# Kernel tuning notes

Hardware: AMD Instinct MI355X
Metric: run time of the kernel (lower is better)

The kernel has to match this reference:

```python
import jax, jax.numpy as jnp
import numpy as np

N, Lq, Lk = 4, 4096, 4096
H, P = 16, 128
D = H * P  # 2048


def setup_inputs() -> dict:
    key = jax.random.key(0)
    ks = jax.random.split(key, 7)
    s = 1.0 / np.sqrt(D).astype(np.float32)
    query = jax.random.normal(ks[0], (N, Lq, D), jnp.float32)
    key_t = jax.random.normal(ks[1], (N, Lk, D), jnp.float32)
    Wq = jax.random.normal(ks[2], (D, D), jnp.float32) * s
    Wk = jax.random.normal(ks[3], (D, D), jnp.float32) * s
    Wv = jax.random.normal(ks[4], (D, D), jnp.float32) * s
    query_padding_mask = jax.random.uniform(ks[5], (N, Lq)) < 0.1
    key_padding_mask = jax.random.uniform(ks[6], (N, Lk)) < 0.1
    return {"query": query, "key": key_t, "Wq": Wq, "Wk": Wk, "Wv": Wv,
            "query_padding_mask": query_padding_mask,
            "key_padding_mask": key_padding_mask}


def reference(query, key, Wq, Wk, Wv, query_padding_mask, key_padding_mask):
    n, lq, _ = query.shape
    lk = key.shape[1]
    # torch.nn.Linear(bias=False): y = x @ W^T; split into heads -> (N,H,L,P)
    q = (query @ Wq.T).reshape(n, lq, H, P).transpose(0, 2, 1, 3)
    k = (key @ Wk.T).reshape(n, lk, H, P).transpose(0, 2, 1, 3)
    v = (key @ Wv.T).reshape(n, lk, H, P).transpose(0, 2, 1, 3)
    # _log_exp_kernel(x) = log(1 + exp(x)) = softplus
    pq = jax.nn.softplus(q)
    pk = jax.nn.softplus(k)
    # zero out padded keys so they contribute nothing to numerator/denominator
    pk = jnp.where(key_padding_mask[:, None, :, None], 0.0, pk)
    # linear attention: O(L*d^2) instead of O(L^2*d)
    kv = jnp.einsum("nhkd,nhke->nhde", pk, v)          # (N,H,P,P)
    num = jnp.einsum("nhqd,nhde->nhqe", pq, kv)        # (N,H,Lq,P)
    den = jnp.einsum("nhqd,nhd->nhq", pq, pk.sum(axis=2))[..., None]
    att = num / den
    out = att.transpose(0, 2, 1, 3).reshape(n, lq, H * P)
    # zero out padded query positions
    out = jnp.where(query_padding_mask[..., None], 0.0, out)
    return out
```

## Files before the change

kernel.cpp:

```cpp
#include <hip/hip_runtime.h>
#include <stdint.h>

typedef __attribute__((ext_vector_type(8))) short    bh8;
typedef __attribute__((ext_vector_type(4))) float    fx4;
typedef __attribute__((ext_vector_type(4))) float    f4v;
typedef unsigned short u16;
typedef __attribute__((ext_vector_type(4))) unsigned short u16x4;

#define DEV static __device__ __forceinline__

DEV u16 f2bf(float f) {
  unsigned u = __float_as_uint(f);
  u += 0x7FFFu + ((u >> 16) & 1u);
  return (u16)(u >> 16);
}
DEV float bf2f(u16 s) { return __uint_as_float(((unsigned)s) << 16); }
DEV float softplus_f(float x) { return fmaxf(x, 0.f) + log1pf(expf(-fabsf(x))); }

DEV void gload_lds16(const u16* g, u16* l) {
  __builtin_amdgcn_global_load_lds(
      (const __attribute__((address_space(1))) unsigned int*)g,
      (__attribute__((address_space(3))) unsigned int*)l, 16, 0, 0);
}
DEV void stage2(const u16* s, u16* d) {
  gload_lds16(s, d);
  gload_lds16(s + 131072, d + 4096);
}

__global__ __launch_bounds__(256) void k_cvt(const float* __restrict__ in,
                                             u16* __restrict__ out, int n4) {
  int i = blockIdx.x * 256 + threadIdx.x;
  int stride = gridDim.x * 256;
  for (; i < n4; i += stride) {
    f4v v = ((const f4v*)in)[i];
    u16x4 o;
    o.x = f2bf(v.x); o.y = f2bf(v.y); o.z = f2bf(v.z); o.w = f2bf(v.w);
    ((u16x4*)out)[i] = o;
  }
}


#define MM(a, b, c) __builtin_amdgcn_mfma_f32_16x16x32_bf16(a, b, c, 0, 0, 0)
#define LD(BASE, RR, KS) \
  (*(const bh8*)&lsg[(BASE) + (RR) * 64 + ((((KS) * 32) + ko8) ^ swz)])

#define DECLQ(Q)                                                          \
  fx4 acc##Q##00 = {}, acc##Q##01 = {}, acc##Q##10 = {}, acc##Q##11 = {}, \
      acc##Q##20 = {}, acc##Q##21 = {}, acc##Q##30 = {}, acc##Q##31 = {}

#define WL asm volatile("s_waitcnt lgkmcnt(0)")
#define WV asm volatile("s_waitcnt vmcnt(4)"); asm volatile("s_waitcnt lgkmcnt(0)")

#define LDA4(AB, KS)                                                     \
  a_0##KS = LD(AB, arow0,      KS); a_1##KS = LD(AB, arow0 + 16, KS);    \
  a_2##KS = LD(AB, arow0 + 32, KS); a_3##KS = LD(AB, arow0 + 48, KS);

#define LDB2(BN, BB, KS)                                                 \
  b##BN##_0##KS = LD(BB, brow0,      KS);                                \
  b##BN##_1##KS = LD(BB, brow0 + 16, KS);

#define MFMA8(Q, BN, KS)                                                 \
  acc##Q##00 = MM(a_0##KS, b##BN##_0##KS, acc##Q##00);                   \
  acc##Q##01 = MM(a_0##KS, b##BN##_1##KS, acc##Q##01);                   \
  acc##Q##10 = MM(a_1##KS, b##BN##_0##KS, acc##Q##10);                   \
  acc##Q##11 = MM(a_1##KS, b##BN##_1##KS, acc##Q##11);                   \
  acc##Q##20 = MM(a_2##KS, b##BN##_0##KS, acc##Q##20);                   \
  acc##Q##21 = MM(a_2##KS, b##BN##_1##KS, acc##Q##21);                   \
  acc##Q##30 = MM(a_3##KS, b##BN##_0##KS, acc##Q##30);                   \
  acc##Q##31 = MM(a_3##KS, b##BN##_1##KS, acc##Q##31);

#define PHASE(MFMAS, WAITS, SSRC, SDST, ...) {  \
  __VA_ARGS__                                   \
  stage2(SSRC, SDST);                           \
  __builtin_amdgcn_s_barrier();                 \
  __builtin_amdgcn_s_setprio(1);                \
  MFMAS                                         \
  __builtin_amdgcn_s_setprio(0);                \
  WAITS;                                        \
  __builtin_amdgcn_s_barrier();                 \
}

#define STE(AC, EL, JOFF) {                                                   \
  float v = AC.EL;                                                            \
  if (EPI >= 1) v = softplus_f(v);                                            \
  if (EPI == 2) { if (mask[gi0 + JOFF]) v = 0.f; }                            \
  C[(size_t)(gi0 + JOFF) * 2048 + gj] = f2bf(v);                              \
}
#define ST1(AC, QR, QC, MI, NI) {                                             \
  int gi0 = bm0 + (QR) * 128 + wr * 64 + (MI) * 16 + (lane >> 4) * 4;         \
  int gj  = bn0 + (QC) * 128 + wc * 32 + (NI) * 16 + l15;                     \
  STE(AC, x, 0) STE(AC, y, 1) STE(AC, z, 2) STE(AC, w, 3)                     \
}
#define EPIQ(Q, QR, QC)                                                       \
  ST1(acc##Q##00, QR, QC, 0, 0) ST1(acc##Q##01, QR, QC, 0, 1)                 \
  ST1(acc##Q##10, QR, QC, 1, 0) ST1(acc##Q##11, QR, QC, 1, 1)                 \
  ST1(acc##Q##20, QR, QC, 2, 0) ST1(acc##Q##21, QR, QC, 2, 1)                 \
  ST1(acc##Q##30, QR, QC, 3, 0) ST1(acc##Q##31, QR, QC, 3, 1)

template <int EPI>
__global__ __launch_bounds__(512, 2) void k_gemm256(
    const u16* __restrict__ A, const u16* __restrict__ B, u16* __restrict__ C,
    const int* __restrict__ mask) {
  extern __shared__ u16 lsg[];
  int tid = threadIdx.x, lane = tid & 63, wid = tid >> 6;
  int xcd = blockIdx.x & 7, i = blockIdx.x >> 3;
  int bm0 = (xcd * 8 + (i & 7)) << 8;
  int bn0 = (i >> 3) << 8;
  int wr = wid >> 2, wc = wid & 3;
  int l15 = lane & 15, ko8 = (lane >> 4) * 8;
  int swz = (l15 & 7) << 3;
  int arow0 = wr * 64 + l15, brow0 = wc * 32 + l15;
  int lr = lane >> 3, cg = (lane & 7) ^ lr;
  const u16* srcA = A + (size_t)(bm0 + wid * 8 + lr) * 2048 + cg * 8;
  const u16* srcB = B + (size_t)(bn0 + wid * 8 + lr) * 2048 + cg * 8;
  u16* lsu = lsg + wid * 512;

  DECLQ(0); DECLQ(1); DECLQ(2); DECLQ(3);
  bh8 a_00 = {}, a_01 = {}, a_10 = {}, a_11 = {},
      a_20 = {}, a_21 = {}, a_30 = {}, a_31 = {};
  bh8 b0_00 = {}, b0_01 = {}, b0_10 = {}, b0_11 = {};
  bh8 b1_00 = {}, b1_01 = {}, b1_10 = {}, b1_11 = {};

  stage2(srcA, lsu + 0);
  stage2(srcB, lsu + 16384);
  stage2(srcA + 262144, lsu + 8192);
  stage2(srcB + 262144, lsu + 24576);
  stage2(srcA + 64, lsu + 32768);
  stage2(srcB + 64, lsu + 49152);
  asm volatile("s_waitcnt vmcnt(4)");
  __builtin_amdgcn_s_barrier();

  for (int it = 0; it < 16; it++) {
    int t1 = 2 * it + 1;
    int t2 = (2 * it + 2) & 31;
    int t3 = (2 * it + 3) & 31;
    PHASE(MFMA8(0, 0, 0) MFMA8(1, 1, 0), WL,
          srcA + 262144 + t1 * 64, lsu + 40960,
          LDA4(0, 0) LDB2(0, 16384, 0) LDB2(1, 24576, 0))
    PHASE(MFMA8(0, 0, 1) MFMA8(1, 1, 1), WL,
          srcB + 262144 + t1 * 64, lsu + 57344,
          LDA4(0, 1) LDB2(0, 16384, 1) LDB2(1, 24576, 1))
    PHASE(MFMA8(2, 0, 0) MFMA8(3, 1, 0), WL,
          srcA + t2 * 64, lsu + 0,
          LDA4(8192, 0))
    PHASE(MFMA8(2, 0, 1) MFMA8(3, 1, 1), WV,
          srcB + t2 * 64, lsu + 16384,
          LDA4(8192, 1))
    PHASE(MFMA8(0, 0, 0) MFMA8(1, 1, 0), WL,
          srcA + 262144 + t2 * 64, lsu + 8192,
          LDA4(32768, 0) LDB2(0, 49152, 0) LDB2(1, 57344, 0))
    PHASE(MFMA8(0, 0, 1) MFMA8(1, 1, 1), WL,
          srcB + 262144 + t2 * 64, lsu + 24576,
          LDA4(32768, 1) LDB2(0, 49152, 1) LDB2(1, 57344, 1))
    PHASE(MFMA8(2, 0, 0) MFMA8(3, 1, 0), WL,
          srcA + t3 * 64, lsu + 32768,
          LDA4(40960, 0))
    PHASE(MFMA8(2, 0, 1) MFMA8(3, 1, 1), WV,
          srcB + t3 * 64, lsu + 49152,
          LDA4(40960, 1))
  }

  EPIQ(0, 0, 0)
  EPIQ(1, 0, 1)
  EPIQ(2, 1, 0)
  EPIQ(3, 1, 1)
}

__global__ __launch_bounds__(256, 2) void k_kv2(const u16* __restrict__ pk,
                                                const u16* __restrict__ v,
                                                float* __restrict__ part,
                                                float* __restrict__ spart) {
  int nh = blockIdx.x >> 3, slab = blockIdx.x & 7;
  int n = nh >> 4, h = nh & 15;
  __shared__ u16 lsA[128 * 32];
  __shared__ u16 lsB[128 * 32];
  __shared__ float redS[32][128];
  int tid = threadIdx.x, lane = tid & 63, wid = tid >> 6;
  int wr = wid >> 1, wc = wid & 1;
  int kk = tid >> 3;
  int dg = (tid & 7) * 16;
  size_t rowbase = ((size_t)(n * 4096 + slab * 512) + kk) * 2048 + h * 128 + dg;
  int r = lane & 15, ko = (lane >> 4) * 8;
  fx4 acc[4][4] = {};
  float sA[16];
#pragma unroll
  for (int i = 0; i < 16; i++) sA[i] = 0.f;
  for (int k0 = 0; k0 < 512; k0 += 32) {
    __syncthreads();
    bh8 a0 = *(const bh8*)(pk + rowbase + (size_t)k0 * 2048);
    bh8 a1 = *(const bh8*)(pk + rowbase + (size_t)k0 * 2048 + 8);
    bh8 b0 = *(const bh8*)(v + rowbase + (size_t)k0 * 2048);
    bh8 b1 = *(const bh8*)(v + rowbase + (size_t)k0 * 2048 + 8);
#pragma unroll
    for (int i = 0; i < 8; i++) {
      sA[i] += bf2f((u16)a0[i]);
      sA[8 + i] += bf2f((u16)a1[i]);
    }
#pragma unroll
    for (int i = 0; i < 8; i++) {
      lsA[(dg + i) * 32 + kk] = (u16)a0[i];
      lsA[(dg + 8 + i) * 32 + kk] = (u16)a1[i];
      lsB[(dg + i) * 32 + kk] = (u16)b0[i];
      lsB[(dg + 8 + i) * 32 + kk] = (u16)b1[i];
    }
    __syncthreads();
    bh8 af[4], bfr[4];
#pragma unroll
    for (int mi = 0; mi < 4; mi++)
      af[mi] = *(const bh8*)&lsA[(wr * 64 + mi * 16 + r) * 32 + ko];
#pragma unroll
    for (int ni = 0; ni < 4; ni++)
      bfr[ni] = *(const bh8*)&lsB[(wc * 64 + ni * 16 + r) * 32 + ko];
#pragma unroll
    for (int mi = 0; mi < 4; mi++)
#pragma unroll
      for (int ni = 0; ni < 4; ni++)
        acc[mi][ni] = __builtin_amdgcn_mfma_f32_16x16x32_bf16(af[mi], bfr[ni],
                                                              acc[mi][ni], 0, 0, 0);
  }
#pragma unroll
  for (int mi = 0; mi < 4; mi++)
#pragma unroll
    for (int ni = 0; ni < 4; ni++)
#pragma unroll
      for (int j = 0; j < 4; j++) {
        int d = wr * 64 + mi * 16 + (lane >> 4) * 4 + j;
        int e = wc * 64 + ni * 16 + (lane & 15);
        part[(size_t)blockIdx.x * 16384 + e * 128 + d] = acc[mi][ni][j];
      }
#pragma unroll
  for (int i = 0; i < 16; i++) redS[kk][dg + i] = sA[i];
  __syncthreads();
  if (tid < 128) {
    float s = 0.f;
#pragma unroll
    for (int p = 0; p < 32; p++) s += redS[p][tid];
    spart[blockIdx.x * 128 + tid] = s;
  }
}

__global__ __launch_bounds__(256) void k_red(const float* __restrict__ part,
                                             const float* __restrict__ spart,
                                             u16* __restrict__ kvT,
                                             float* __restrict__ sb) {
  int nh = blockIdx.x, tid = threadIdx.x;
  for (int i = tid; i < 16384; i += 256) {
    float s = 0.f;
#pragma unroll
    for (int sl = 0; sl < 8; sl++) s += part[(size_t)(nh * 8 + sl) * 16384 + i];
    kvT[(size_t)nh * 16384 + i] = f2bf(s);
  }
  if (tid < 128) {
    float s = 0.f;
#pragma unroll
    for (int sl = 0; sl < 8; sl++) s += spart[(nh * 8 + sl) * 128 + tid];
    sb[nh * 128 + tid] = s;
  }
}

__global__ __launch_bounds__(256, 2) void k_att(
    const u16* __restrict__ pq, const u16* __restrict__ kvT,
    const float* __restrict__ s, const int* __restrict__ qmask,
    float* __restrict__ out) {
  int b = blockIdx.x;
  int lt = b & 31, h = (b >> 5) & 15, nb = b >> 9;
  int l0 = lt * 128;
  __shared__ u16 lsQ[128 * 128];
  __shared__ u16 lsKV[128 * 128];
  __shared__ float lsS[128];
  __shared__ float lsDen[128];
  int tid = threadIdx.x, lane = tid & 63, wid = tid >> 6;

  int row = tid >> 1, part = tid & 1;
  const u16* gq = pq + ((size_t)(nb * 4096 + l0 + row)) * 2048 + h * 128 + part * 64;
  const u16* gk = kvT + ((size_t)(nb * 16 + h) * 128 + row) * 128 + part * 64;
  int sw = (row & 7) << 3;
#pragma unroll
  for (int j = 0; j < 8; j++) {
    bh8 vq = *(const bh8*)(gq + j * 8);
    bh8 vk = *(const bh8*)(gk + j * 8);
    int ci = (part * 64 + j * 8) ^ sw;
    *(bh8*)&lsQ[row * 128 + ci] = vq;
    *(bh8*)&lsKV[row * 128 + ci] = vk;
  }
  if (tid < 128) lsS[tid] = s[(nb * 16 + h) * 128 + tid];
  __syncthreads();

  if (tid < 128) {
    int rr = tid, swr = (rr & 7) << 3;
    float dsum = 0.f;
    for (int dd = 0; dd < 128; dd++) {
      int d = (dd + rr) & 127;
      dsum += bf2f(lsQ[rr * 128 + (d ^ swr)]) * lsS[d];
    }
    lsDen[rr] = dsum;
  }
  __syncthreads();

  int wr = wid >> 1, wc = wid & 1;
  int r = lane & 15, ko = (lane >> 4) * 8;
  fx4 acc[4][4] = {};
#pragma unroll
  for (int ks = 0; ks < 4; ks++) {
    bh8 af[4], bfr[4];
#pragma unroll
    for (int mi = 0; mi < 4; mi++) {
      int rw = wr * 64 + mi * 16 + r;
      af[mi] = *(const bh8*)&lsQ[rw * 128 + ((ks * 32 + ko) ^ ((rw & 7) << 3))];
    }
#pragma unroll
    for (int ni = 0; ni < 4; ni++) {
      int rw = wc * 64 + ni * 16 + r;
      bfr[ni] = *(const bh8*)&lsKV[rw * 128 + ((ks * 32 + ko) ^ ((rw & 7) << 3))];
    }
#pragma unroll
    for (int mi = 0; mi < 4; mi++)
#pragma unroll
      for (int ni = 0; ni < 4; ni++)
        acc[mi][ni] = __builtin_amdgcn_mfma_f32_16x16x32_bf16(af[mi], bfr[ni],
                                                              acc[mi][ni], 0, 0, 0);
  }
#pragma unroll
  for (int mi = 0; mi < 4; mi++)
#pragma unroll
    for (int ni = 0; ni < 4; ni++)
#pragma unroll
      for (int j = 0; j < 4; j++) {
        int li = wr * 64 + mi * 16 + (lane >> 4) * 4 + j;
        int e = wc * 64 + ni * 16 + (lane & 15);
        int l = l0 + li;
        float v = qmask[nb * 4096 + l] ? 0.f : acc[mi][ni][j] / lsDen[li];
        out[((size_t)(nb * 4096 + l)) * 2048 + h * 128 + e] = v;
      }
}

extern "C" void kernel_launch(void* const* d_in, const int* in_sizes, int n_in,
                              void* d_out, int out_size, void* d_ws, size_t ws_size,
                              hipStream_t stream) {
  const float* query = (const float*)d_in[0];
  const float* key   = (const float*)d_in[1];
  const float* Wq    = (const float*)d_in[2];
  const float* Wk    = (const float*)d_in[3];
  const float* Wv    = (const float*)d_in[4];
  const int* qmask   = (const int*)d_in[5];
  const int* kmask   = (const int*)d_in[6];
  float* out = (float*)d_out;
  char* ws = (char*)d_ws;

  u16* qb   = (u16*)(ws + 0);
  u16* kb   = (u16*)(ws + 67108864ull);
  u16* Wqb  = (u16*)(ws + 134217728ull);
  u16* Wkb  = (u16*)(ws + 142606336ull);
  u16* Wvb  = (u16*)(ws + 150994944ull);
  u16* pq   = (u16*)(ws + 159383552ull);
  u16* kvT  = (u16*)(ws + 226492416ull);
  float* sb = (float*)(ws + 228589568ull);
  float* kvpart = (float*)(ws + 0);
  float* spart  = (float*)(ws + 33554432ull);
  u16* pk = (u16*)d_out;
  u16* vb = (u16*)d_out + 33554432ull;

  k_cvt<<<2048, 256, 0, stream>>>(query, qb, 33554432 / 4);
  k_cvt<<<2048, 256, 0, stream>>>(key, kb, 33554432 / 4);
  k_cvt<<<512, 256, 0, stream>>>(Wq, Wqb, 4194304 / 4);
  k_cvt<<<512, 256, 0, stream>>>(Wk, Wkb, 4194304 / 4);
  k_cvt<<<512, 256, 0, stream>>>(Wv, Wvb, 4194304 / 4);

  k_gemm256<1><<<512, 512, 131072, stream>>>(qb, Wqb, pq, nullptr);
  k_gemm256<2><<<512, 512, 131072, stream>>>(kb, Wkb, pk, kmask);
  k_gemm256<0><<<512, 512, 131072, stream>>>(kb, Wvb, vb, nullptr);

  k_kv2<<<512, 256, 0, stream>>>(pk, vb, kvpart, spart);
  k_red<<<64, 256, 0, stream>>>(kvpart, spart, kvT, sb);
  k_att<<<2048, 256, 0, stream>>>(pq, kvT, sb, qmask, out);
}
```

Measured before the change: 739.1 us.

## Software-pipeline LDS fragment loads one phase ahead of MFMAs in GEMM

Restructures the 8-phase GEMM main loop so each phase issues the LDS fragment reads for the next phase's MFMAs, and moves the global-to-LDS staging into reordered slots. The per-phase lgkmcnt(0) waits are dropped and replaced by vmcnt(6)/vmcnt(4) waits on global loads. The prologue now stages an extra tile and preloads the first fragments. The aim is to hide LDS read latency behind MFMA execution. The cost is more live fragment registers and a tighter buffer-reuse schedule that is hard to verify for races.

Result: no change. 741.5 us (+0.3%).

```diff
diff --git a/kernel.cpp b/kernel.cpp
--- a/kernel.cpp
+++ b/kernel.cpp
@@ -48,8 +48,9 @@
   fx4 acc##Q##00 = {}, acc##Q##01 = {}, acc##Q##10 = {}, acc##Q##11 = {}, \
       acc##Q##20 = {}, acc##Q##21 = {}, acc##Q##30 = {}, acc##Q##31 = {}
 
-#define WL asm volatile("s_waitcnt lgkmcnt(0)")
-#define WV asm volatile("s_waitcnt vmcnt(4)"); asm volatile("s_waitcnt lgkmcnt(0)")
+#define WN
+#define WV6 asm volatile("s_waitcnt vmcnt(6)");
+#define WV4 asm volatile("s_waitcnt vmcnt(4)");
 
 #define LDA4(AB, KS)                                                     \
   a_0##KS = LD(AB, arow0,      KS); a_1##KS = LD(AB, arow0 + 16, KS);    \
@@ -69,14 +70,13 @@
   acc##Q##30 = MM(a_3##KS, b##BN##_0##KS, acc##Q##30);                   \
   acc##Q##31 = MM(a_3##KS, b##BN##_1##KS, acc##Q##31);
 
-#define PHASE(MFMAS, WAITS, SSRC, SDST, ...) {  \
+#define PH(MFMAS, WAITS, ...) {                 \
   __VA_ARGS__                                   \
-  stage2(SSRC, SDST);                           \
   __builtin_amdgcn_s_barrier();                 \
   __builtin_amdgcn_s_setprio(1);                \
   MFMAS                                         \
   __builtin_amdgcn_s_setprio(0);                \
-  WAITS;                                        \
+  WAITS                                         \
   __builtin_amdgcn_s_barrier();                 \
 }
 
@@ -123,41 +123,39 @@
 
   stage2(srcA, lsu + 0);
   stage2(srcB, lsu + 16384);
+  stage2(srcB + 262144, lsu + 24576);
   stage2(srcA + 262144, lsu + 8192);
-  stage2(srcB + 262144, lsu + 24576);
   stage2(srcA + 64, lsu + 32768);
   stage2(srcB + 64, lsu + 49152);
-  asm volatile("s_waitcnt vmcnt(4)");
+  stage2(srcB + 262144 + 64, lsu + 57344);
+  asm volatile("s_waitcnt vmcnt(8)");
   __builtin_amdgcn_s_barrier();
+  LDA4(0, 0) LDB2(0, 16384, 0) LDB2(1, 24576, 0)
 
   for (int it = 0; it < 16; it++) {
     int t1 = 2 * it + 1;
     int t2 = (2 * it + 2) & 31;
     int t3 = (2 * it + 3) & 31;
-    PHASE(MFMA8(0, 0, 0) MFMA8(1, 1, 0), WL,
-          srcA + 262144 + t1 * 64, lsu + 40960,
-          LDA4(0, 0) LDB2(0, 16384, 0) LDB2(1, 24576, 0))
-    PHASE(MFMA8(0, 0, 1) MFMA8(1, 1, 1), WL,
-          srcB + 262144 + t1 * 64, lsu + 57344,
-          LDA4(0, 1) LDB2(0, 16384, 1) LDB2(1, 24576, 1))
-    PHASE(MFMA8(2, 0, 0) MFMA8(3, 1, 0), WL,
-          srcA + t2 * 64, lsu + 0,
-          LDA4(8192, 0))
-    PHASE(MFMA8(2, 0, 1) MFMA8(3, 1, 1), WV,
-          srcB + t2 * 64, lsu + 16384,
-          LDA4(8192, 1))
-    PHASE(MFMA8(0, 0, 0) MFMA8(1, 1, 0), WL,
-          srcA + 262144 + t2 * 64, lsu + 8192,
-          LDA4(32768, 0) LDB2(0, 49152, 0) LDB2(1, 57344, 0))
-    PHASE(MFMA8(0, 0, 1) MFMA8(1, 1, 1), WL,
-          srcB + 262144 + t2 * 64, lsu + 24576,
-          LDA4(32768, 1) LDB2(0, 49152, 1) LDB2(1, 57344, 1))
-    PHASE(MFMA8(2, 0, 0) MFMA8(3, 1, 0), WL,
-          srcA + t3 * 64, lsu + 32768,
-          LDA4(40960, 0))
-    PHASE(MFMA8(2, 0, 1) MFMA8(3, 1, 1), WV,
-          srcB + t3 * 64, lsu + 49152,
-          LDA4(40960, 1))
+    PH(MFMA8(0, 0, 0) MFMA8(1, 1, 0), WV6,
+       LDA4(0, 1) LDB2(0, 16384, 1) LDB2(1, 24576, 1))
+    PH(MFMA8(0, 0, 1) MFMA8(1, 1, 1), WN,
+       LDA4(8192, 0) stage2(srcA + 262144 + t1 * 64, lsu + 40960);)
+    PH(MFMA8(2, 0, 0) MFMA8(3, 1, 0), WV4,
+       LDA4(8192, 1) stage2(srcA + t2 * 64, lsu + 0);)
+    PH(MFMA8(2, 0, 1) MFMA8(3, 1, 1), WN,
+       LDA4(32768, 0) LDB2(0, 49152, 0) LDB2(1, 57344, 0)
+       stage2(srcB + t2 * 64, lsu + 16384);)
+    PH(MFMA8(0, 0, 0) MFMA8(1, 1, 0), WV6,
+       LDA4(32768, 1) LDB2(0, 49152, 1) LDB2(1, 57344, 1)
+       stage2(srcB + 262144 + t2 * 64, lsu + 24576);)
+    PH(MFMA8(0, 0, 1) MFMA8(1, 1, 1), WN,
+       LDA4(40960, 0) stage2(srcA + 262144 + t2 * 64, lsu + 8192);)
+    PH(MFMA8(2, 0, 0) MFMA8(3, 1, 0), WV6,
+       LDA4(40960, 1) stage2(srcA + t3 * 64, lsu + 32768);
+       stage2(srcB + t3 * 64, lsu + 49152);)
+    PH(MFMA8(2, 0, 1) MFMA8(3, 1, 1), WN,
+       LDA4(0, 0) LDB2(0, 16384, 0) LDB2(1, 24576, 0)
+       stage2(srcB + 262144 + t3 * 64, lsu + 57344);)
   }
 
   EPIQ(0, 0, 0)
```
